# Kernel optimization log

Measured on AMD Instinct MI355X. Metric: run time of the kernel, lower is better.

## Reference

```python
import jax, jax.numpy as jnp
import numpy as np

H = 8          # num_attention_heads
HEAD_DIM = 24  # 192 / 8


def setup_inputs() -> dict:
    key = jax.random.key(0)
    k1, k2, k3 = jax.random.split(key, 3)
    B, S, D = 4, 2048, 192
    x = jax.random.normal(k1, (B, S, D), dtype=jnp.float32)
    mask0 = jnp.zeros((B, 1, 1, S), dtype=jnp.float32)  # HF additive attention mask
    w_attn = jax.random.normal(k2, (D, 3 * D), dtype=jnp.float32) * 0.02
    b_attn = jnp.zeros((3 * D,), dtype=jnp.float32)
    w_proj = jax.random.normal(k3, (D, D), dtype=jnp.float32) * 0.02
    b_proj = jnp.zeros((D,), dtype=jnp.float32)
    return {"x": x, "mask0": mask0, "w_attn": w_attn, "b_attn": b_attn,
            "w_proj": w_proj, "b_proj": b_proj}


def reference(x, mask0, w_attn, b_attn, w_proj, b_proj):
    B, S, D = x.shape
    # fused QKV projection (GPT2 Conv1D: x @ W + b)
    qkv = x @ w_attn + b_attn                       # [B,S,3D]
    q, k, v = jnp.split(qkv, 3, axis=-1)
    def split_heads(t):
        return t.reshape(B, S, H, HEAD_DIM).transpose(0, 2, 1, 3)  # [B,H,S,hd]
    q, k, v = split_heads(q), split_heads(k), split_heads(v)
    # scaled QK^T
    scores = jnp.einsum('bhqd,bhkd->bhqk', q, k) / jnp.sqrt(
        jnp.asarray(HEAD_DIM, dtype=q.dtype))
    # causal mask (masked_fill with dtype min), then additive padding mask
    causal = jnp.tril(jnp.ones((S, S), dtype=bool))
    mask_value = jnp.finfo(scores.dtype).min
    scores = jnp.where(causal, scores, mask_value) + mask0
    attn = jax.nn.softmax(scores, axis=-1)          # [B,H,S,S]
    # attn_dropout is identity in eval mode
    out = jnp.einsum('bhqk,bhkd->bhqd', attn, v)    # [B,H,S,hd]
    out = out.transpose(0, 2, 1, 3).reshape(B, S, D)
    return out @ w_proj + b_proj
```

## Files before the change

kernel.cpp:

```cpp
#include <hip/hip_runtime.h>

typedef unsigned short u16;
typedef unsigned int u32;
typedef __bf16 bf16x8 __attribute__((ext_vector_type(8)));
typedef float f32x4 __attribute__((ext_vector_type(4)));
typedef float f32x16 __attribute__((ext_vector_type(16)));
typedef u32 u32x2 __attribute__((ext_vector_type(2)));
typedef u32 u32x4 __attribute__((ext_vector_type(4)));

#define NB 4
#define NS 2048
#define ND 192
#define NH 8
#define HD 24
#define NM (NB*NS)
#define N3 (3*ND)

#define LOG2E 1.4426950408889634f
#define QSCALE (0.20412414523193152f * 1.4426950408889634f)

__device__ __forceinline__ u16 f2bf(float f){
  union { float f; unsigned u; } a; a.f = f;
  unsigned r = a.u + 0x7fffu + ((a.u >> 16) & 1u);
  return (u16)(r >> 16);
}

__device__ __forceinline__ u32 cvtpk(float lo, float hi){
  u32 r; asm("v_cvt_pk_bf16_f32 %0, %1, %2" : "=v"(r) : "v"(lo), "v"(hi)); return r;
}
__device__ __forceinline__ void pswap(u32 &a, u32 &b){
  asm("v_permlane32_swap_b32 %0, %1" : "+v"(a), "+v"(b));
}

__device__ __forceinline__ void transpose64(
    const float* __restrict__ src, int srcN, u16* __restrict__ dst, int dstK,
    int k0, int n0, u16 (*sh)[68], int tid)
{
  int r = tid >> 2, cs = tid & 3;
  const float* sp = src + (size_t)(k0 + r)*srcN + n0 + cs*16;
  #pragma unroll
  for (int q = 0; q < 4; ++q) {
    float4 v = *(const float4*)(sp + q*4);
    u16 o[4] = { f2bf(v.x), f2bf(v.y), f2bf(v.z), f2bf(v.w) };
    *(u32x2*)&sh[r][cs*16 + q*4] = *(const u32x2*)o;
  }
  __syncthreads();
  int n = tid >> 2, ks = tid & 3;
  u16 tmp[16];
  #pragma unroll
  for (int j = 0; j < 16; ++j) tmp[j] = sh[ks*16 + j][n];
  u16* dp = dst + (size_t)(n0 + n)*dstK + k0 + ks*16;
  *(u32x4*)dp       = *(const u32x4*)tmp;
  *(u32x4*)(dp + 8) = *(const u32x4*)(tmp + 8);
}

__global__ __launch_bounds__(256) void prep_kernel(
    const float* __restrict__ x, const float* __restrict__ w_attn,
    const float* __restrict__ w_proj, const float* __restrict__ mask0,
    u16* __restrict__ xb, u16* __restrict__ wta, u16* __restrict__ wtp,
    u16* __restrict__ qp, u16* __restrict__ kp)
{
  __shared__ u16 sh[64][68];
  const int bid = blockIdx.x, tid = threadIdx.x;
  if (bid < 1536) {
    int i = bid*256 + tid;
    float4 v = reinterpret_cast<const float4*>(x)[i];
    u16 o[4] = { f2bf(v.x), f2bf(v.y), f2bf(v.z), f2bf(v.w) };
    *reinterpret_cast<u32x2*>(xb + (size_t)i*4) = *(const u32x2*)o;
  } else if (bid < 1536 + 27) {
    int t = bid - 1536; int kt = t/9, nt = t%9;
    transpose64(w_attn, N3, wta, ND, kt*64, nt*64, sh, tid);
  } else if (bid < 1536 + 27 + 9) {
    int t = bid - 1563; int kt = t/3, nt = t%3;
    transpose64(w_proj, ND, wtp, ND, kt*64, nt*64, sh, tid);
  } else {
    int i = (bid - 1572)*256 + tid;
    int sg = i >> 3, h = i & 7;
    int b = sg >> 11, s = sg & (NS-1);
    size_t base = ((size_t)((b*NS + s)*NH + h))*32 + 24;
    qp[base] = 0x3F80;
    kp[base] = f2bf(mask0[b*NS + s] * LOG2E);
  }
}

__global__ __launch_bounds__(256) void qkv_kernel(
    const u16* __restrict__ xb, const u16* __restrict__ wta,
    const float* __restrict__ b_attn,
    u16* __restrict__ qp, u16* __restrict__ kp, u16* __restrict__ vtp)
{
  __shared__ u16 tile[64][104];
  const int m0 = blockIdx.x*64, n0 = blockIdx.y*96;
  const int tid = threadIdx.x;
  const int w = tid >> 6, lane = tid & 63, c = lane & 15, g = lane >> 4;
  f32x4 acc[6] = {};
  const int ar = m0 + w*16 + c;
  #pragma unroll
  for (int ks = 0; ks < 6; ++ks) {
    bf16x8 af = *(const bf16x8*)(xb + (size_t)ar*ND + ks*32 + g*8);
    #pragma unroll
    for (int t = 0; t < 6; ++t) {
      bf16x8 bfr = *(const bf16x8*)(wta + (size_t)(n0 + t*16 + c)*ND + ks*32 + g*8);
      acc[t] = __builtin_amdgcn_mfma_f32_16x16x32_bf16(af, bfr, acc[t], 0, 0, 0);
    }
  }
  const int b = m0 >> 11, sb = m0 & (NS-1);
  if (n0 >= 384) {
    #pragma unroll
    for (int t = 0; t < 6; ++t) {
      int n = n0 + t*16 + c, nv = n - 384;
      int hv = nv / HD, dv = nv % HD;
      float bias = b_attn[n];
      u16 o4[4];
      #pragma unroll
      for (int r = 0; r < 4; ++r) o4[r] = f2bf(acc[t][r] + bias);
      size_t idx = ((size_t)((b*NH + hv)*32 + dv))*NS + sb + w*16 + g*4;
      *(u32x2*)(vtp + idx) = *(const u32x2*)o4;
    }
  } else {
    const float scl = (n0 < 192) ? QSCALE : 1.0f;
    #pragma unroll
    for (int t = 0; t < 6; ++t) {
      float bias = b_attn[n0 + t*16 + c];
      #pragma unroll
      for (int r = 0; r < 4; ++r)
        tile[w*16 + g*4 + r][t*16 + c] = f2bf((acc[t][r] + bias)*scl);
    }
    __syncthreads();
    int row = tid >> 2, run = tid & 3;
    int hq = ((n0 % 192) / HD) + run;
    u16* dst = ((n0 < 192) ? qp : kp)
             + ((size_t)((b*NS + sb + row)*NH + hq))*32;
    const u16* src = &tile[row][run*24];
    *(u32x4*)(dst)      = *(const u32x4*)(src);
    *(u32x4*)(dst + 8)  = *(const u32x4*)(src + 8);
    *(u32x4*)(dst + 16) = *(const u32x4*)(src + 16);
  }
}

__global__ __launch_bounds__(64) void attn_kernel(
    const u16* __restrict__ qp, const u16* __restrict__ kp,
    const u16* __restrict__ vtp, u16* __restrict__ ao)
{
  __shared__ u16 ot[32][36];
  const int qt = 63 - (int)blockIdx.x;
  const int bh = blockIdx.y;
  const int b = bh >> 3, h = bh & 7;
  const int lane = threadIdx.x, c = lane & 31, hi = lane >> 5;
  const int q0 = qt*32;

  const size_t rowstride = NH*32;
  const size_t qkbase = (size_t)b*NS*rowstride + h*32;
  const size_t vbase  = ((size_t)(bh*32 + c))*NS;

  const u16* qrow = qp + qkbase + (size_t)(q0 + c)*rowstride;
  bf16x8 qf0 = *(const bf16x8*)(qrow + hi*8);
  bf16x8 qf1 = *(const bf16x8*)(qrow + 16 + hi*8);

  f32x16 o = {0};
  const f32x16 z16 = {0};
  float m = 0.f, l = 0.f;

  const u16* k0row = kp + qkbase + (size_t)c*rowstride;
  bf16x8 ka0 = *(const bf16x8*)(k0row + hi*8);
  bf16x8 ka1 = *(const bf16x8*)(k0row + 16 + hi*8);
  bf16x8 va0 = *(const bf16x8*)(vtp + vbase + hi*8);
  bf16x8 va1 = *(const bf16x8*)(vtp + vbase + 16 + hi*8);

  for (int jt = 0; jt <= qt; ++jt) {
    const int k0 = jt*32;
    const int kn = (jt < qt) ? k0 + 32 : k0;
    const u16* knrow = kp + qkbase + (size_t)(kn + c)*rowstride;
    bf16x8 kb0 = *(const bf16x8*)(knrow + hi*8);
    bf16x8 kb1 = *(const bf16x8*)(knrow + 16 + hi*8);
    bf16x8 vb0 = *(const bf16x8*)(vtp + vbase + kn + hi*8);
    bf16x8 vb1 = *(const bf16x8*)(vtp + vbase + kn + 16 + hi*8);

    f32x16 st = __builtin_amdgcn_mfma_f32_32x32x16_bf16(ka0, qf0, z16, 0, 0, 0);
    st        = __builtin_amdgcn_mfma_f32_32x32x16_bf16(ka1, qf1, st,  0, 0, 0);

    float pm = -3.0e38f;
    if (jt == qt) {
      #pragma unroll
      for (int r = 0; r < 16; ++r) {
        int krel = (r & 3) + 8*(r >> 2) + 4*hi;
        float s = (k0 + krel > q0 + c) ? -3.0e38f : st[r];
        st[r] = s; pm = fmaxf(pm, s);
      }
    } else {
      #pragma unroll
      for (int r = 0; r < 16; ++r) pm = fmaxf(pm, st[r]);
    }

    if (!__all(pm - m <= 8.f)) {
      float pm2 = fmaxf(pm, __shfl_xor(pm, 32));
      float mn = fmaxf(m, pm2);
      float al = __builtin_amdgcn_exp2f(m - mn);
      #pragma unroll
      for (int r = 0; r < 16; ++r) o[r] *= al;
      l *= al; m = mn;
    }

    float ls = 0.f;
    #pragma unroll
    for (int r = 0; r < 16; ++r) {
      float p = __builtin_amdgcn_exp2f(st[r] - m);
      st[r] = p; ls += p;
    }
    l += ls;

    u32 a0 = cvtpk(st[0], st[1]),  b0 = cvtpk(st[4], st[5]);
    u32 a1 = cvtpk(st[2], st[3]),  b1 = cvtpk(st[6], st[7]);
    pswap(a0, b0); pswap(a1, b1);
    u32 a2 = cvtpk(st[8], st[9]),  b2 = cvtpk(st[12], st[13]);
    u32 a3 = cvtpk(st[10], st[11]), b3 = cvtpk(st[14], st[15]);
    pswap(a2, b2); pswap(a3, b3);
    union { u32 w[4]; bf16x8 v; } pf0, pf1;
    pf0.w[0] = a0; pf0.w[1] = a1; pf0.w[2] = b0; pf0.w[3] = b1;
    pf1.w[0] = a2; pf1.w[1] = a3; pf1.w[2] = b2; pf1.w[3] = b3;

    o = __builtin_amdgcn_mfma_f32_32x32x16_bf16(va0, pf0.v, o, 0, 0, 0);
    o = __builtin_amdgcn_mfma_f32_32x32x16_bf16(va1, pf1.v, o, 0, 0, 0);

    ka0 = kb0; ka1 = kb1; va0 = vb0; va1 = vb1;
  }

  float lt = l + __shfl_xor(l, 32);
  float inv = 1.0f / lt;
  #pragma unroll
  for (int r = 0; r < 16; ++r) {
    int d = (r & 3) + 8*(r >> 2) + 4*hi;
    if (d < HD) ot[c][d] = f2bf(o[r]*inv);
  }
  __syncthreads();
  int q = lane >> 1, half = lane & 1;
  const u16* src = &ot[q][half*12];
  u32x2 w0 = *(const u32x2*)src;
  u32x2 w1 = *(const u32x2*)(src + 4);
  u32x2 w2 = *(const u32x2*)(src + 8);
  u16* dst = ao + ((size_t)(b*NS + q0 + q))*ND + h*HD + half*12;
  *(u32x2*)dst       = w0;
  *(u32x2*)(dst + 4) = w1;
  *(u32x2*)(dst + 8) = w2;
}

__global__ __launch_bounds__(256) void proj_kernel(
    const u16* __restrict__ ao, const u16* __restrict__ wtp,
    const float* __restrict__ bp, float* __restrict__ out)
{
  const int m0 = blockIdx.x*64, n0 = blockIdx.y*64;
  const int tid = threadIdx.x;
  const int w = tid >> 6, lane = tid & 63, c = lane & 15, g = lane >> 4;
  f32x4 acc[4] = {};
  const int ar = m0 + w*16 + c;
  #pragma unroll
  for (int ks = 0; ks < 6; ++ks) {
    bf16x8 af = *(const bf16x8*)(ao + (size_t)ar*ND + ks*32 + g*8);
    #pragma unroll
    for (int t = 0; t < 4; ++t) {
      bf16x8 bfr = *(const bf16x8*)(wtp + (size_t)(n0 + t*16 + c)*ND + ks*32 + g*8);
      acc[t] = __builtin_amdgcn_mfma_f32_16x16x32_bf16(af, bfr, acc[t], 0, 0, 0);
    }
  }
  #pragma unroll
  for (int t = 0; t < 4; ++t) {
    int n = n0 + t*16 + c;
    float bias = bp[n];
    #pragma unroll
    for (int r = 0; r < 4; ++r) {
      int mm = m0 + w*16 + g*4 + r;
      out[(size_t)mm*ND + n] = acc[t][r] + bias;
    }
  }
}

extern "C" void kernel_launch(void* const* d_in, const int* in_sizes, int n_in,
                              void* d_out, int out_size, void* d_ws, size_t ws_size,
                              hipStream_t stream)
{
  const float* x      = (const float*)d_in[0];
  const float* mask0  = (const float*)d_in[1];
  const float* w_attn = (const float*)d_in[2];
  const float* b_attn = (const float*)d_in[3];
  const float* w_proj = (const float*)d_in[4];
  const float* b_proj = (const float*)d_in[5];
  float* out = (float*)d_out;

  char* ws = (char*)d_ws;
  u16* qp  = (u16*)(ws);
  u16* kp  = (u16*)(ws + ((size_t)4  << 20));
  u16* vtp = (u16*)(ws + ((size_t)8  << 20));
  u16* xb  = (u16*)(ws + ((size_t)12 << 20));
  u16* wta = (u16*)(ws + ((size_t)15 << 20));
  u16* wtp = (u16*)(ws + ((size_t)15 << 20) + 256*1024);
  u16* ao  = (u16*)(ws + ((size_t)15 << 20) + 512*1024);

  hipMemsetAsync(ws, 0, (size_t)8 << 20, stream);

  prep_kernel<<<1828, 256, 0, stream>>>(x, w_attn, w_proj, mask0,
                                        xb, wta, wtp, qp, kp);
  qkv_kernel<<<dim3(NM/64, 6), 256, 0, stream>>>(xb, wta, b_attn, qp, kp, vtp);
  attn_kernel<<<dim3(64, NB*NH), 64, 0, stream>>>(qp, kp, vtp, ao);
  proj_kernel<<<dim3(NM/64, ND/64), 256, 0, stream>>>(ao, wtp, b_proj, out);
}
```

Measured before the change: 160.9 us.

## Split attention KV range in two with a merge kernel, drop workspace memset

The attention kernel now splits each query tile's key range into two halves across a new grid dimension. Each half writes unnormalized bf16 partial outputs plus its running max, and a new merge kernel combines them with log-sum-exp weights and normalizes. The row sum is carried in the padded V column (a ones row written by the qkv kernel), so the separate l accumulation is removed. The qkv kernel now writes the Q/K padding columns and mask directly, replacing the prep padding pass and the 8MB memset. This doubles the block count to fill the GPU better at the cost of an extra launch, extra partial-result traffic, and bf16 rounding of the partial sums.

```diff
diff --git a/kernel.cpp b/kernel.cpp
--- a/kernel.cpp
+++ b/kernel.cpp
@@ -15,6 +15,8 @@
 #define HD 24
 #define NM (NB*NS)
 #define N3 (3*ND)
+#define NBH (NB*NH)
+#define NROWS (NBH*NS)
 
 #define LOG2E 1.4426950408889634f
 #define QSCALE (0.20412414523193152f * 1.4426950408889634f)
@@ -24,7 +26,9 @@
   unsigned r = a.u + 0x7fffu + ((a.u >> 16) & 1u);
   return (u16)(r >> 16);
 }
-
+__device__ __forceinline__ float b2f(u16 h){
+  union { u32 u; float f; } a; a.u = ((u32)h) << 16; return a.f;
+}
 __device__ __forceinline__ u32 cvtpk(float lo, float hi){
   u32 r; asm("v_cvt_pk_bf16_f32 %0, %1, %2" : "=v"(r) : "v"(lo), "v"(hi)); return r;
 }
@@ -56,9 +60,8 @@
 
 __global__ __launch_bounds__(256) void prep_kernel(
     const float* __restrict__ x, const float* __restrict__ w_attn,
-    const float* __restrict__ w_proj, const float* __restrict__ mask0,
-    u16* __restrict__ xb, u16* __restrict__ wta, u16* __restrict__ wtp,
-    u16* __restrict__ qp, u16* __restrict__ kp)
+    const float* __restrict__ w_proj,
+    u16* __restrict__ xb, u16* __restrict__ wta, u16* __restrict__ wtp)
 {
   __shared__ u16 sh[64][68];
   const int bid = blockIdx.x, tid = threadIdx.x;
@@ -70,25 +73,18 @@
   } else if (bid < 1536 + 27) {
     int t = bid - 1536; int kt = t/9, nt = t%9;
     transpose64(w_attn, N3, wta, ND, kt*64, nt*64, sh, tid);
-  } else if (bid < 1536 + 27 + 9) {
+  } else {
     int t = bid - 1563; int kt = t/3, nt = t%3;
     transpose64(w_proj, ND, wtp, ND, kt*64, nt*64, sh, tid);
-  } else {
-    int i = (bid - 1572)*256 + tid;
-    int sg = i >> 3, h = i & 7;
-    int b = sg >> 11, s = sg & (NS-1);
-    size_t base = ((size_t)((b*NS + s)*NH + h))*32 + 24;
-    qp[base] = 0x3F80;
-    kp[base] = f2bf(mask0[b*NS + s] * LOG2E);
   }
 }
 
 __global__ __launch_bounds__(256) void qkv_kernel(
     const u16* __restrict__ xb, const u16* __restrict__ wta,
-    const float* __restrict__ b_attn,
+    const float* __restrict__ b_attn, const float* __restrict__ mask0,
     u16* __restrict__ qp, u16* __restrict__ kp, u16* __restrict__ vtp)
 {
-  __shared__ u16 tile[64][104];
+  __shared__ u16 tile[96*72];
   const int m0 = blockIdx.x*64, n0 = blockIdx.y*96;
   const int tid = threadIdx.x;
   const int w = tid >> 6, lane = tid & 63, c = lane & 15, g = lane >> 4;
@@ -105,48 +101,86 @@
   }
   const int b = m0 >> 11, sb = m0 & (NS-1);
   if (n0 >= 384) {
-    #pragma unroll
-    for (int t = 0; t < 6; ++t) {
-      int n = n0 + t*16 + c, nv = n - 384;
-      int hv = nv / HD, dv = nv % HD;
-      float bias = b_attn[n];
-      u16 o4[4];
-      #pragma unroll
-      for (int r = 0; r < 4; ++r) o4[r] = f2bf(acc[t][r] + bias);
-      size_t idx = ((size_t)((b*NH + hv)*32 + dv))*NS + sb + w*16 + g*4;
-      *(u32x2*)(vtp + idx) = *(const u32x2*)o4;
-    }
-  } else {
-    const float scl = (n0 < 192) ? QSCALE : 1.0f;
+    const int h0 = (n0 - 384)/HD;
     #pragma unroll
     for (int t = 0; t < 6; ++t) {
       float bias = b_attn[n0 + t*16 + c];
       #pragma unroll
       for (int r = 0; r < 4; ++r)
-        tile[w*16 + g*4 + r][t*16 + c] = f2bf((acc[t][r] + bias)*scl);
+        tile[(t*16 + c)*72 + w*16 + g*4 + r] = f2bf(acc[t][r] + bias);
+    }
+    __syncthreads();
+    if (tid < 200) {
+      int row = tid >> 1, seg = tid & 1;
+      if (row < 96) {
+        int hl = row / HD, dv = row % HD;
+        u16* dst = vtp + ((size_t)((b*NH + h0 + hl)*32 + dv))*NS + sb + seg*32;
+        const u16* src = &tile[row*72 + seg*32];
+        #pragma unroll
+        for (int q = 0; q < 4; ++q)
+          *(u32x4*)(dst + q*8) = *(const u32x4*)(src + q*8);
+      } else {
+        int hl = row - 96;
+        u16* dst = vtp + ((size_t)((b*NH + h0 + hl)*32 + 24))*NS + sb + seg*32;
+        u16 ones[8] = {0x3F80,0x3F80,0x3F80,0x3F80,0x3F80,0x3F80,0x3F80,0x3F80};
+        #pragma unroll
+        for (int q = 0; q < 4; ++q)
+          *(u32x4*)(dst + q*8) = *(const u32x4*)ones;
+      }
+    }
+  } else {
+    const bool isQ = (n0 < 192);
+    const float scl = isQ ? QSCALE : 1.0f;
+    #pragma unroll
+    for (int t = 0; t < 6; ++t) {
+      float bias = b_attn[n0 + t*16 + c];
+      #pragma unroll
+      for (int r = 0; r < 4; ++r)
+        tile[(w*16 + g*4 + r)*104 + t*16 + c] = f2bf((acc[t][r] + bias)*scl);
     }
     __syncthreads();
     int row = tid >> 2, run = tid & 3;
-    int hq = ((n0 % 192) / HD) + run;
-    u16* dst = ((n0 < 192) ? qp : kp)
-             + ((size_t)((b*NS + sb + row)*NH + hq))*32;
-    const u16* src = &tile[row][run*24];
-    *(u32x4*)(dst)      = *(const u32x4*)(src);
-    *(u32x4*)(dst + 8)  = *(const u32x4*)(src + 8);
-    *(u32x4*)(dst + 16) = *(const u32x4*)(src + 16);
+    int h0 = (n0 % 192)/HD;
+    u16 d24 = isQ ? (u16)0x3F80
+                  : f2bf(mask0[b*NS + sb + row] * LOG2E);
+    u16 buf[32];
+    #pragma unroll
+    for (int j = 0; j < 24; ++j) buf[j] = tile[row*104 + run*24 + j];
+    buf[24] = d24;
+    #pragma unroll
+    for (int j = 25; j < 32; ++j) buf[j] = 0;
+    u16* dst = (isQ ? qp : kp)
+             + ((size_t)((b*NS + sb + row)*NH + h0 + run))*32;
+    #pragma unroll
+    for (int q = 0; q < 4; ++q)
+      *(u32x4*)(dst + q*8) = *(const u32x4*)(buf + q*8);
   }
 }
 
 __global__ __launch_bounds__(64) void attn_kernel(
     const u16* __restrict__ qp, const u16* __restrict__ kp,
-    const u16* __restrict__ vtp, u16* __restrict__ ao)
-{
-  __shared__ u16 ot[32][36];
+    const u16* __restrict__ vtp, u16* __restrict__ po, float* __restrict__ pmf)
+{
   const int qt = 63 - (int)blockIdx.x;
   const int bh = blockIdx.y;
+  const int part = blockIdx.z;
   const int b = bh >> 3, h = bh & 7;
   const int lane = threadIdx.x, c = lane & 31, hi = lane >> 5;
   const int q0 = qt*32;
+  const int nt = qt + 1, halfn = (nt + 1) >> 1;
+  const int t0 = part ? halfn : 0;
+  const int t1 = part ? nt : halfn;
+
+  const int pidx = part*NROWS + bh*NS + q0 + c;
+  u16* porow = po + (size_t)pidx*32;
+
+  if (t0 >= t1) {
+    u32x2 z = {0,0};
+    #pragma unroll
+    for (int rr = 0; rr < 4; ++rr) *(u32x2*)(porow + rr*8 + hi*4) = z;
+    if (hi == 0) pmf[pidx] = -3.0e38f;
+    return;
+  }
 
   const size_t rowstride = NH*32;
   const size_t qkbase = (size_t)b*NS*rowstride + h*32;
@@ -158,17 +192,17 @@
 
   f32x16 o = {0};
   const f32x16 z16 = {0};
-  float m = 0.f, l = 0.f;
-
-  const u16* k0row = kp + qkbase + (size_t)c*rowstride;
+  float m = 0.f;
+
+  const u16* k0row = kp + qkbase + (size_t)(t0*32 + c)*rowstride;
   bf16x8 ka0 = *(const bf16x8*)(k0row + hi*8);
   bf16x8 ka1 = *(const bf16x8*)(k0row + 16 + hi*8);
-  bf16x8 va0 = *(const bf16x8*)(vtp + vbase + hi*8);
-  bf16x8 va1 = *(const bf16x8*)(vtp + vbase + 16 + hi*8);
-
-  for (int jt = 0; jt <= qt; ++jt) {
+  bf16x8 va0 = *(const bf16x8*)(vtp + vbase + t0*32 + hi*8);
+  bf16x8 va1 = *(const bf16x8*)(vtp + vbase + t0*32 + 16 + hi*8);
+
+  for (int jt = t0; jt < t1; ++jt) {
     const int k0 = jt*32;
-    const int kn = (jt < qt) ? k0 + 32 : k0;
+    const int kn = ((jt + 1 < t1) ? jt + 1 : jt)*32;
     const u16* knrow = kp + qkbase + (size_t)(kn + c)*rowstride;
     bf16x8 kb0 = *(const bf16x8*)(knrow + hi*8);
     bf16x8 kb1 = *(const bf16x8*)(knrow + 16 + hi*8);
@@ -197,16 +231,12 @@
       float al = __builtin_amdgcn_exp2f(m - mn);
       #pragma unroll
       for (int r = 0; r < 16; ++r) o[r] *= al;
-      l *= al; m = mn;
-    }
-
-    float ls = 0.f;
-    #pragma unroll
-    for (int r = 0; r < 16; ++r) {
-      float p = __builtin_amdgcn_exp2f(st[r] - m);
-      st[r] = p; ls += p;
-    }
-    l += ls;
+      m = mn;
+    }
+
+    #pragma unroll
+    for (int r = 0; r < 16; ++r)
+      st[r] = __builtin_amdgcn_exp2f(st[r] - m);
 
     u32 a0 = cvtpk(st[0], st[1]),  b0 = cvtpk(st[4], st[5]);
     u32 a1 = cvtpk(st[2], st[3]),  b1 = cvtpk(st[6], st[7]);
@@ -224,23 +254,45 @@
     ka0 = kb0; ka1 = kb1; va0 = vb0; va1 = vb1;
   }
 
-  float lt = l + __shfl_xor(l, 32);
-  float inv = 1.0f / lt;
-  #pragma unroll
-  for (int r = 0; r < 16; ++r) {
-    int d = (r & 3) + 8*(r >> 2) + 4*hi;
-    if (d < HD) ot[c][d] = f2bf(o[r]*inv);
-  }
-  __syncthreads();
-  int q = lane >> 1, half = lane & 1;
-  const u16* src = &ot[q][half*12];
-  u32x2 w0 = *(const u32x2*)src;
-  u32x2 w1 = *(const u32x2*)(src + 4);
-  u32x2 w2 = *(const u32x2*)(src + 8);
-  u16* dst = ao + ((size_t)(b*NS + q0 + q))*ND + h*HD + half*12;
-  *(u32x2*)dst       = w0;
-  *(u32x2*)(dst + 4) = w1;
-  *(u32x2*)(dst + 8) = w2;
+  #pragma unroll
+  for (int rr = 0; rr < 4; ++rr) {
+    u32 lo = cvtpk(o[rr*4 + 0], o[rr*4 + 1]);
+    u32 hi2 = cvtpk(o[rr*4 + 2], o[rr*4 + 3]);
+    u32x2 wv = {lo, hi2};
+    *(u32x2*)(porow + rr*8 + hi*4) = wv;
+  }
+  if (hi == 0) pmf[pidx] = m;
+}
+
+__global__ __launch_bounds__(256) void merge_kernel(
+    const u16* __restrict__ po, const float* __restrict__ pmf,
+    u16* __restrict__ ao)
+{
+  int i = blockIdx.x*256 + threadIdx.x;
+  int bh = i >> 11, q = i & (NS-1);
+  int b = bh >> 3, h = bh & 7;
+  float m1 = pmf[i], m2 = pmf[NROWS + i];
+  float M = fmaxf(m1, m2);
+  float w1 = __builtin_amdgcn_exp2f(m1 - M);
+  float w2 = __builtin_amdgcn_exp2f(m2 - M);
+  const u16* r1 = po + (size_t)i*32;
+  const u16* r2 = r1 + (size_t)NROWS*32;
+  u16 a1[32], a2[32];
+  #pragma unroll
+  for (int q4 = 0; q4 < 4; ++q4) {
+    *(u32x4*)(a1 + q4*8) = *(const u32x4*)(r1 + q4*8);
+    *(u32x4*)(a2 + q4*8) = *(const u32x4*)(r2 + q4*8);
+  }
+  float l = b2f(a1[24])*w1 + b2f(a2[24])*w2;
+  float inv = 1.0f / l;
+  u16 ob[24];
+  #pragma unroll
+  for (int d = 0; d < 24; ++d)
+    ob[d] = f2bf((b2f(a1[d])*w1 + b2f(a2[d])*w2)*inv);
+  u16* dst = ao + ((size_t)(b*NS + q))*ND + h*HD;
+  #pragma unroll
+  for (int q4 = 0; q4 < 3; ++q4)
+    *(u32x4*)(dst + q4*8) = *(const u32x4*)(ob + q4*8);
 }
 
 __global__ __launch_bounds__(256) void proj_kernel(
@@ -286,19 +338,20 @@
   float* out = (float*)d_out;
 
   char* ws = (char*)d_ws;
-  u16* qp  = (u16*)(ws);
-  u16* kp  = (u16*)(ws + ((size_t)4  << 20));
-  u16* vtp = (u16*)(ws + ((size_t)8  << 20));
-  u16* xb  = (u16*)(ws + ((size_t)12 << 20));
-  u16* wta = (u16*)(ws + ((size_t)15 << 20));
-  u16* wtp = (u16*)(ws + ((size_t)15 << 20) + 256*1024);
-  u16* ao  = (u16*)(ws + ((size_t)15 << 20) + 512*1024);
-
-  hipMemsetAsync(ws, 0, (size_t)8 << 20, stream);
-
-  prep_kernel<<<1828, 256, 0, stream>>>(x, w_attn, w_proj, mask0,
-                                        xb, wta, wtp, qp, kp);
-  qkv_kernel<<<dim3(NM/64, 6), 256, 0, stream>>>(xb, wta, b_attn, qp, kp, vtp);
-  attn_kernel<<<dim3(64, NB*NH), 64, 0, stream>>>(qp, kp, vtp, ao);
+  u16*   qp  = (u16*)(ws);
+  u16*   kp  = (u16*)(ws + ((size_t)4  << 20));
+  u16*   vtp = (u16*)(ws + ((size_t)8  << 20));
+  u16*   xb  = (u16*)(ws + ((size_t)12 << 20));
+  u16*   wta = (u16*)(ws + ((size_t)15 << 20));
+  u16*   wtp = (u16*)(ws + ((size_t)15 << 20) + 256*1024);
+  u16*   ao  = (u16*)(ws + ((size_t)15 << 20) + 512*1024);
+  u16*   po  = (u16*)(ws + ((size_t)18 << 20) + 512*1024);
+  float* pmf = (float*)(ws + ((size_t)26 << 20) + 512*1024);
+
+  prep_kernel<<<1572, 256, 0, stream>>>(x, w_attn, w_proj, xb, wta, wtp);
+  qkv_kernel<<<dim3(NM/64, 6), 256, 0, stream>>>(xb, wta, b_attn, mask0,
+                                                 qp, kp, vtp);
+  attn_kernel<<<dim3(64, NBH, 2), 64, 0, stream>>>(qp, kp, vtp, po, pmf);
+  merge_kernel<<<256, 256, 0, stream>>>(po, pmf, ao);
   proj_kernel<<<dim3(NM/64, ND/64), 256, 0, stream>>>(ao, wtp, b_proj, out);
 }
```

Result: slower. 164.4 us (+2.2%).
